# Optimization experiments

Hardware: AMD Instinct MI355X
Metric: run time of the kernel (lower is better)

The kernel has to match this reference:

```python
import jax, jax.numpy as jnp
import numpy as np

HEAD_SIZE = 64

def setup_inputs() -> dict:
    key = jax.random.key(0)
    k1, k2, k3, k4 = jax.random.split(key, 4)
    B, T, D = 4, 4096, 768
    x = jax.random.normal(k1, (B, T, D), dtype=jnp.float32)
    Wq = jax.random.normal(k2, (D, HEAD_SIZE), dtype=jnp.float32) * (1.0 / np.sqrt(D))
    Wk = jax.random.normal(k3, (D, HEAD_SIZE), dtype=jnp.float32) * (1.0 / np.sqrt(D))
    Wv = jax.random.normal(k4, (D, HEAD_SIZE), dtype=jnp.float32) * (1.0 / np.sqrt(D))
    return {"x": x, "Wq": Wq, "Wk": Wk, "Wv": Wv}

def reference(x, Wq, Wk, Wv):
    # q,k,v: [B, T, H]
    q = jnp.einsum('btd,dh->bth', x, Wq)
    k = jnp.einsum('btd,dh->bth', x, Wk)
    v = jnp.einsum('btd,dh->bth', x, Wv)
    # scores: [B, T, T]; causal mask via lower-triangular band, -inf elsewhere
    scores = jnp.einsum('bqh,bkh->bqk', q, k)
    T = x.shape[1]
    causal = jnp.tril(jnp.ones((T, T), dtype=bool))  # band_part(ones, -1, 0)
    scores = jnp.where(causal[None, :, :], scores, -jnp.inf)
    attn = jax.nn.softmax(scores / np.sqrt(HEAD_SIZE), axis=-1)
    # dropout is identity in eval mode
    return jnp.einsum('bqk,bkh->bqh', attn, v)
```

## Files before the change

### kernel.cpp

```cpp
#include <hip/hip_runtime.h>
#include <math.h>

typedef __attribute__((ext_vector_type(8))) short short8;
typedef __attribute__((ext_vector_type(4))) float f32x4;
typedef unsigned short ushort_t;

#define TSEQ   4096
#define NBATCH 4
#define DMODEL 768
#define HS     64

static __device__ __forceinline__ ushort_t f2bf(float f) {
  union { float f; unsigned u; } v; v.f = f;
  unsigned r = v.u + 0x7fffu + ((v.u >> 16) & 1u);
  return (ushort_t)(r >> 16);
}
static __device__ __forceinline__ float bf2f(ushort_t u) {
  union { unsigned u; float f; } v; v.u = ((unsigned)u) << 16; return v.f;
}

#define MFMA16(a,b,c) __builtin_amdgcn_mfma_f32_16x16x32_bf16((a),(b),(c),0,0,0)

__global__ __launch_bounds__(256) void wprep(
    const float* __restrict__ Wq, const float* __restrict__ Wk,
    const float* __restrict__ Wv, ushort_t* __restrict__ Wt)
{
  __shared__ float lds[64 * 65];
  const int m = blockIdx.x / 12, kc = blockIdx.x % 12, k0 = kc * 64;
  const float* W = (m == 0) ? Wq : (m == 1) ? Wk : Wv;
  const int tid = threadIdx.x;
#pragma unroll
  for (int i = 0; i < 16; i++) {
    const int row = i * 4 + (tid >> 6), col = tid & 63;
    lds[row * 65 + col] = W[(size_t)(k0 + row) * HS + col];
  }
  __syncthreads();
#pragma unroll
  for (int i = 0; i < 16; i++) {
    const int n = i * 4 + (tid >> 6), kk = tid & 63;
    Wt[(size_t)(m * 64 + n) * DMODEL + k0 + kk] = f2bf(lds[kk * 65 + n]);
  }
}

__global__ __launch_bounds__(512) void qkv_mfma(
    const float* __restrict__ x, const ushort_t* __restrict__ Wt,
    ushort_t* __restrict__ q, ushort_t* __restrict__ kO, ushort_t* __restrict__ vT)
{
  __shared__ __align__(16) ushort_t Abuf[2][64 * 72];

  const int tid  = threadIdx.x;
  const int w    = tid >> 6, lane = tid & 63;
  const int l16  = lane & 15, quad = lane >> 4;
  const int mh   = w >> 1, ns = w & 1;
  const int M0   = blockIdx.x * 64;
  const float* xg = x + (size_t)M0 * DMODEL;

  const int srow = tid >> 3, scol = (tid & 7) * 8;
  const float* xs = xg + (size_t)srow * DMODEL + scol;
  const ushort_t* wb = Wt + (size_t)(ns * 96 + l16) * DMODEL + quad * 8;

  f32x4 acc[6];
#pragma unroll
  for (int nt = 0; nt < 6; nt++) acc[nt] = (f32x4){0.f, 0.f, 0.f, 0.f};

  float4 pr0 = *(const float4*)(xs);
  float4 pr1 = *(const float4*)(xs + 4);
  short8 bpre[12];
#pragma unroll
  for (int nt = 0; nt < 6; nt++)
#pragma unroll
    for (int kc = 0; kc < 2; kc++)
      bpre[nt * 2 + kc] = *(const short8*)(wb + (size_t)nt * 16 * DMODEL + kc * 32);

  for (int ks = 0; ks < DMODEL / 64; ks++) {
    ushort_t* Ab = &Abuf[ks & 1][0];
    {
      short8 p;
      p[0]=f2bf(pr0.x); p[1]=f2bf(pr0.y); p[2]=f2bf(pr0.z); p[3]=f2bf(pr0.w);
      p[4]=f2bf(pr1.x); p[5]=f2bf(pr1.y); p[6]=f2bf(pr1.z); p[7]=f2bf(pr1.w);
      *(short8*)(Ab + srow * 72 + scol) = p;
    }
    if (ks < DMODEL / 64 - 1) {
      const float* xn = xs + (ks + 1) * 64;
      pr0 = *(const float4*)(xn);
      pr1 = *(const float4*)(xn + 4);
    }
    __syncthreads();
    short8 bcur[12];
#pragma unroll
    for (int t = 0; t < 12; t++) bcur[t] = bpre[t];
    if (ks < DMODEL / 64 - 1) {
#pragma unroll
      for (int nt = 0; nt < 6; nt++)
#pragma unroll
        for (int kc = 0; kc < 2; kc++)
          bpre[nt * 2 + kc] =
              *(const short8*)(wb + (size_t)nt * 16 * DMODEL + (ks + 1) * 64 + kc * 32);
    }
#pragma unroll
    for (int kc = 0; kc < 2; kc++) {
      const short8 af = *(const short8*)(Ab + (mh * 16 + l16) * 72 + kc * 32 + quad * 8);
#pragma unroll
      for (int nt = 0; nt < 6; nt++) acc[nt] = MFMA16(af, bcur[nt * 2 + kc], acc[nt]);
    }
  }

#pragma unroll
  for (int nt = 0; nt < 6; nt++) {
    const int gnt = ns * 6 + nt;
    const int mat = gnt >> 2;
    if (mat <= 1) {
      const int col = (gnt & 3) * 16 + l16;
#pragma unroll
      for (int r = 0; r < 4; r++) {
        const float val = acc[nt][r];
        const int trow = M0 + mh * 16 + quad * 4 + r;
        if (mat == 0) q [(size_t)trow * HS + col] = f2bf(val * 0.125f);
        else          kO[(size_t)trow * HS + col] = f2bf(val);
      }
    }
  }
  __syncthreads();
  float* vls = (float*)&Abuf[0][0];
  if (ns == 1) {
#pragma unroll
    for (int nt = 2; nt < 6; nt++) {
      const int vcol = ((ns * 6 + nt) & 3) * 16 + l16;
#pragma unroll
      for (int r = 0; r < 4; r++)
        vls[(mh * 16 + quad * 4 + r) * 65 + vcol] = acc[nt][r];
    }
  }
  __syncthreads();
  const int d = tid >> 3, seg = tid & 7;
  short8 pk;
#pragma unroll
  for (int i = 0; i < 8; i++) pk[i] = (short)f2bf(vls[(seg * 8 + i) * 65 + d]);
  *(short8*)(vT + ((size_t)(M0 >> 12) * HS + d) * TSEQ + (M0 & (TSEQ - 1)) + seg * 8) = pk;
}

#define KP 72
__global__ __launch_bounds__(128) void attn_part(
    const ushort_t* __restrict__ q, const ushort_t* __restrict__ k,
    const ushort_t* __restrict__ vT, float* __restrict__ ML, ushort_t* __restrict__ OP)
{
  __shared__ __align__(16) ushort_t sK[64 * KP];
  __shared__ __align__(16) ushort_t sV[64 * KP];
  __shared__ __align__(16) ushort_t sP[2][16 * KP];

  const int idx  = blockIdx.x;
  const int s    = idx & 1;
  const int b    = (idx >> 1) & 3;
  const int jt   = 127 - (idx >> 3);
  const int tid  = threadIdx.x;
  const int w    = tid >> 6;
  const int lane = tid & 63;
  const int l16  = lane & 15, quad = lane >> 4;
  const int R0   = jt * 32 + w * 16;

  const ushort_t* qg = q  + (size_t)b * TSEQ * HS;
  const ushort_t* kg = k  + (size_t)b * TSEQ * HS;
  const ushort_t* vg = vT + (size_t)b * HS * TSEQ;

  const short8 qf0 = *(const short8*)(qg + (R0 + l16) * HS +      quad * 8);
  const short8 qf1 = *(const short8*)(qg + (R0 + l16) * HS + 32 + quad * 8);

  f32x4 o[4];
#pragma unroll
  for (int dt = 0; dt < 4; dt++) o[dt] = (f32x4){0.f, 0.f, 0.f, 0.f};
  float mrow = -INFINITY, lrow = 0.f;

  const int nkt = jt / 2 + 1;
  short8 kpre[4], vpre[4];
  int kt = s;
  if (kt < nkt) {
    const int k0 = kt * 64;
#pragma unroll
    for (int i = 0; i < 4; i++) {
      const int c = i * 128 + tid, key = c >> 3, ch = c & 7;
      kpre[i] = *(const short8*)(kg + (size_t)(k0 + key) * HS + ch * 8);
      vpre[i] = *(const short8*)(vg + (size_t)key * TSEQ + k0 + ch * 8);
    }
  }
  for (; kt < nkt; kt += 2) {
    const int k0 = kt * 64;
    __syncthreads();
#pragma unroll
    for (int i = 0; i < 4; i++) {
      const int c = i * 128 + tid, key = c >> 3, ch = c & 7;
      *(short8*)(sK + key * KP + ch * 8) = kpre[i];
      *(short8*)(sV + key * KP + ch * 8) = vpre[i];
    }
    if (kt + 2 < nkt) {
      const int kn = (kt + 2) * 64;
#pragma unroll
      for (int i = 0; i < 4; i++) {
        const int c = i * 128 + tid, key = c >> 3, ch = c & 7;
        kpre[i] = *(const short8*)(kg + (size_t)(kn + key) * HS + ch * 8);
        vpre[i] = *(const short8*)(vg + (size_t)key * TSEQ + kn + ch * 8);
      }
    }
    __syncthreads();
    f32x4 sT[4];
#pragma unroll
    for (int ct = 0; ct < 4; ct++) {
      sT[ct] = (f32x4){0.f, 0.f, 0.f, 0.f};
      const short8 kfa = *(const short8*)(sK + (ct * 16 + l16) * KP +      quad * 8);
      const short8 kfb = *(const short8*)(sK + (ct * 16 + l16) * KP + 32 + quad * 8);
      sT[ct] = MFMA16(kfa, qf0, sT[ct]);
      sT[ct] = MFMA16(kfb, qf1, sT[ct]);
    }
    if (k0 + 63 > R0) {
      const int qrow = R0 + l16;
#pragma unroll
      for (int ct = 0; ct < 4; ct++)
#pragma unroll
        for (int r = 0; r < 4; r++)
          sT[ct][r] = (k0 + ct * 16 + quad * 4 + r <= qrow) ? sT[ct][r] : -INFINITY;
    }
    float tm = -INFINITY;
#pragma unroll
    for (int ct = 0; ct < 4; ct++)
#pragma unroll
      for (int r = 0; r < 4; r++) tm = fmaxf(tm, sT[ct][r]);
    tm = fmaxf(tm, __shfl_xor(tm, 16));
    tm = fmaxf(tm, __shfl_xor(tm, 32));
    const float mn = fmaxf(mrow, tm);
    const float al = __expf(mrow - mn);
    mrow = mn;
    float ps = 0.f;
#pragma unroll
    for (int ct = 0; ct < 4; ct++)
#pragma unroll
      for (int r = 0; r < 4; r++) { sT[ct][r] = __expf(sT[ct][r] - mn); ps += sT[ct][r]; }
    ps += __shfl_xor(ps, 16);
    ps += __shfl_xor(ps, 32);
    lrow = lrow * al + ps;
    ushort_t* Pw = &sP[w][0];
#pragma unroll
    for (int ct = 0; ct < 4; ct++) {
      ushort4 pk;
      pk.x = f2bf(sT[ct][0]); pk.y = f2bf(sT[ct][1]);
      pk.z = f2bf(sT[ct][2]); pk.w = f2bf(sT[ct][3]);
      *(ushort4*)(Pw + l16 * KP + ct * 16 + quad * 4) = pk;
    }
    float alo[4];
#pragma unroll
    for (int r = 0; r < 4; r++) alo[r] = __shfl(al, quad * 4 + r);
#pragma unroll
    for (int dt = 0; dt < 4; dt++)
#pragma unroll
      for (int r = 0; r < 4; r++) o[dt][r] *= alo[r];
    const short8 pf0 = *(const short8*)(Pw + l16 * KP +      quad * 8);
    const short8 pf1 = *(const short8*)(Pw + l16 * KP + 32 + quad * 8);
#pragma unroll
    for (int dt = 0; dt < 4; dt++) {
      const short8 vfa = *(const short8*)(sV + (dt * 16 + l16) * KP +      quad * 8);
      const short8 vfb = *(const short8*)(sV + (dt * 16 + l16) * KP + 32 + quad * 8);
      o[dt] = MFMA16(pf0, vfa, o[dt]);
      o[dt] = MFMA16(pf1, vfb, o[dt]);
    }
  }

  const size_t base = ((size_t)(b * 2 + s) * TSEQ);
  if (quad == 0) {
    ML[(base + R0 + l16) * 2 + 0] = mrow;
    ML[(base + R0 + l16) * 2 + 1] = lrow;
  }
#pragma unroll
  for (int dt = 0; dt < 4; dt++)
#pragma unroll
    for (int r = 0; r < 4; r++)
      OP[(base + R0 + quad * 4 + r) * HS + dt * 16 + l16] = f2bf(o[dt][r]);
}

__global__ __launch_bounds__(256) void attn_merge(
    const float* __restrict__ ML, const ushort_t* __restrict__ OP,
    float* __restrict__ out)
{
  const int row = blockIdx.x * 16 + (threadIdx.x >> 4);
  const int b   = row >> 12, t = row & (TSEQ - 1);
  const int d0  = (threadIdx.x & 15) * 4;
  const size_t i0 = ((size_t)(b * 2 + 0) * TSEQ + t);
  const size_t i1 = ((size_t)(b * 2 + 1) * TSEQ + t);
  const float m0 = ML[i0 * 2], l0 = ML[i0 * 2 + 1];
  const float m1 = ML[i1 * 2], l1 = ML[i1 * 2 + 1];
  const float M  = fmaxf(m0, m1);
  const float a0 = __expf(m0 - M), a1 = __expf(m1 - M);
  const float inv = 1.f / (l0 * a0 + l1 * a1);
  const ushort4 u0 = *(const ushort4*)(OP + i0 * HS + d0);
  const ushort4 u1 = *(const ushort4*)(OP + i1 * HS + d0);
  float4 res;
  res.x = (a0 * bf2f(u0.x) + a1 * bf2f(u1.x)) * inv;
  res.y = (a0 * bf2f(u0.y) + a1 * bf2f(u1.y)) * inv;
  res.z = (a0 * bf2f(u0.z) + a1 * bf2f(u1.z)) * inv;
  res.w = (a0 * bf2f(u0.w) + a1 * bf2f(u1.w)) * inv;
  *(float4*)(out + (size_t)row * HS + d0) = res;
}

extern "C" void kernel_launch(void* const* d_in, const int* in_sizes, int n_in,
                              void* d_out, int out_size, void* d_ws, size_t ws_size,
                              hipStream_t stream) {
  const float* x  = (const float*)d_in[0];
  const float* Wq = (const float*)d_in[1];
  const float* Wk = (const float*)d_in[2];
  const float* Wv = (const float*)d_in[3];
  float* out = (float*)d_out;

  char* ws = (char*)d_ws;
  ushort_t* Wt = (ushort_t*)ws;
  ushort_t* qb = (ushort_t*)(ws + 294912);
  ushort_t* kb = (ushort_t*)(ws + 294912 + 2097152);
  ushort_t* vb = (ushort_t*)(ws + 294912 + 2 * 2097152);
  float*    ml = (float*)   (ws + 294912 + 3 * 2097152);
  ushort_t* op = (ushort_t*)(ws + 294912 + 3 * 2097152 + 262144);

  wprep<<<36, 256, 0, stream>>>(Wq, Wk, Wv, Wt);
  qkv_mfma<<<(NBATCH * TSEQ) / 64, 512, 0, stream>>>(x, Wt, qb, kb, vb);
  attn_part<<<1024, 128, 0, stream>>>(qb, kb, vb, ml, op);
  attn_merge<<<1024, 256, 0, stream>>>(ml, op, out);
}
```

Before: 158.8 us.

## Increase attention key-split to four and halve QKV projection tile

The attention partial kernel now splits each query tile's key range four ways instead of two, launching twice as many blocks and widening the merge step to combine four partial (m, l, O) results. The QKV projection kernel uses 32-row tiles with 256 threads and a two-blocks-per-CU launch bound, doubling its grid. The aim is more parallelism and less tail imbalance in the causal attention pass. In exchange it writes and reads more partial output and adds merge traffic.

```diff
diff --git a/kernel.cpp b/kernel.cpp
--- a/kernel.cpp
+++ b/kernel.cpp
@@ -9,6 +9,7 @@
 #define NBATCH 4
 #define DMODEL 768
 #define HS     64
+#define KSPLIT 4
 
 static __device__ __forceinline__ ushort_t f2bf(float f) {
   union { float f; unsigned u; } v; v.f = f;
@@ -42,17 +43,17 @@
   }
 }
 
-__global__ __launch_bounds__(512) void qkv_mfma(
+__global__ __launch_bounds__(256, 2) void qkv_mfma(
     const float* __restrict__ x, const ushort_t* __restrict__ Wt,
     ushort_t* __restrict__ q, ushort_t* __restrict__ kO, ushort_t* __restrict__ vT)
 {
-  __shared__ __align__(16) ushort_t Abuf[2][64 * 72];
+  __shared__ __align__(16) ushort_t Abuf[2][32 * 72];
 
   const int tid  = threadIdx.x;
   const int w    = tid >> 6, lane = tid & 63;
   const int l16  = lane & 15, quad = lane >> 4;
   const int mh   = w >> 1, ns = w & 1;
-  const int M0   = blockIdx.x * 64;
+  const int M0   = blockIdx.x * 32;
   const float* xg = x + (size_t)M0 * DMODEL;
 
   const int srow = tid >> 3, scol = (tid & 7) * 8;
@@ -132,7 +133,7 @@
     }
   }
   __syncthreads();
-  const int d = tid >> 3, seg = tid & 7;
+  const int d = tid >> 2, seg = tid & 3;
   short8 pk;
 #pragma unroll
   for (int i = 0; i < 8; i++) pk[i] = (short)f2bf(vls[(seg * 8 + i) * 65 + d]);
@@ -149,9 +150,9 @@
   __shared__ __align__(16) ushort_t sP[2][16 * KP];
 
   const int idx  = blockIdx.x;
-  const int s    = idx & 1;
-  const int b    = (idx >> 1) & 3;
-  const int jt   = 127 - (idx >> 3);
+  const int s    = idx & 3;
+  const int b    = (idx >> 2) & 3;
+  const int jt   = 127 - (idx >> 4);
   const int tid  = threadIdx.x;
   const int w    = tid >> 6;
   const int lane = tid & 63;
@@ -182,7 +183,7 @@
       vpre[i] = *(const short8*)(vg + (size_t)key * TSEQ + k0 + ch * 8);
     }
   }
-  for (; kt < nkt; kt += 2) {
+  for (; kt < nkt; kt += KSPLIT) {
     const int k0 = kt * 64;
     __syncthreads();
 #pragma unroll
@@ -191,8 +192,8 @@
       *(short8*)(sK + key * KP + ch * 8) = kpre[i];
       *(short8*)(sV + key * KP + ch * 8) = vpre[i];
     }
-    if (kt + 2 < nkt) {
-      const int kn = (kt + 2) * 64;
+    if (kt + KSPLIT < nkt) {
+      const int kn = (kt + KSPLIT) * 64;
 #pragma unroll
       for (int i = 0; i < 4; i++) {
         const int c = i * 128 + tid, key = c >> 3, ch = c & 7;
@@ -262,7 +263,7 @@
     }
   }
 
-  const size_t base = ((size_t)(b * 2 + s) * TSEQ);
+  const size_t base = ((size_t)(b * KSPLIT + s) * TSEQ);
   if (quad == 0) {
     ML[(base + R0 + l16) * 2 + 0] = mrow;
     ML[(base + R0 + l16) * 2 + 1] = lrow;
@@ -281,21 +282,28 @@
   const int row = blockIdx.x * 16 + (threadIdx.x >> 4);
   const int b   = row >> 12, t = row & (TSEQ - 1);
   const int d0  = (threadIdx.x & 15) * 4;
-  const size_t i0 = ((size_t)(b * 2 + 0) * TSEQ + t);
-  const size_t i1 = ((size_t)(b * 2 + 1) * TSEQ + t);
-  const float m0 = ML[i0 * 2], l0 = ML[i0 * 2 + 1];
-  const float m1 = ML[i1 * 2], l1 = ML[i1 * 2 + 1];
-  const float M  = fmaxf(m0, m1);
-  const float a0 = __expf(m0 - M), a1 = __expf(m1 - M);
-  const float inv = 1.f / (l0 * a0 + l1 * a1);
-  const ushort4 u0 = *(const ushort4*)(OP + i0 * HS + d0);
-  const ushort4 u1 = *(const ushort4*)(OP + i1 * HS + d0);
-  float4 res;
-  res.x = (a0 * bf2f(u0.x) + a1 * bf2f(u1.x)) * inv;
-  res.y = (a0 * bf2f(u0.y) + a1 * bf2f(u1.y)) * inv;
-  res.z = (a0 * bf2f(u0.z) + a1 * bf2f(u1.z)) * inv;
-  res.w = (a0 * bf2f(u0.w) + a1 * bf2f(u1.w)) * inv;
-  *(float4*)(out + (size_t)row * HS + d0) = res;
+  float m[KSPLIT], l[KSPLIT];
+  float M = -INFINITY;
+#pragma unroll
+  for (int ss = 0; ss < KSPLIT; ss++) {
+    const size_t i = ((size_t)(b * KSPLIT + ss) * TSEQ + t);
+    m[ss] = ML[i * 2]; l[ss] = ML[i * 2 + 1];
+    M = fmaxf(M, m[ss]);
+  }
+  float den = 0.f;
+  float4 num = make_float4(0.f, 0.f, 0.f, 0.f);
+#pragma unroll
+  for (int ss = 0; ss < KSPLIT; ss++) {
+    const float a = __expf(m[ss] - M);
+    den += l[ss] * a;
+    const size_t i = ((size_t)(b * KSPLIT + ss) * TSEQ + t);
+    const ushort4 u = *(const ushort4*)(OP + i * HS + d0);
+    num.x += a * bf2f(u.x); num.y += a * bf2f(u.y);
+    num.z += a * bf2f(u.z); num.w += a * bf2f(u.w);
+  }
+  const float inv = 1.f / den;
+  *(float4*)(out + (size_t)row * HS + d0) =
+      make_float4(num.x * inv, num.y * inv, num.z * inv, num.w * inv);
 }
 
 extern "C" void kernel_launch(void* const* d_in, const int* in_sizes, int n_in,
@@ -313,10 +321,10 @@
   ushort_t* kb = (ushort_t*)(ws + 294912 + 2097152);
   ushort_t* vb = (ushort_t*)(ws + 294912 + 2 * 2097152);
   float*    ml = (float*)   (ws + 294912 + 3 * 2097152);
-  ushort_t* op = (ushort_t*)(ws + 294912 + 3 * 2097152 + 262144);
+  ushort_t* op = (ushort_t*)(ws + 294912 + 3 * 2097152 + 524288);
 
   wprep<<<36, 256, 0, stream>>>(Wq, Wk, Wv, Wt);
-  qkv_mfma<<<(NBATCH * TSEQ) / 64, 512, 0, stream>>>(x, Wt, qb, kb, vb);
-  attn_part<<<1024, 128, 0, stream>>>(qb, kb, vb, ml, op);
+  qkv_mfma<<<(NBATCH * TSEQ) / 32, 256, 0, stream>>>(x, Wt, qb, kb, vb);
+  attn_part<<<128 * NBATCH * KSPLIT, 128, 0, stream>>>(qb, kb, vb, ml, op);
   attn_merge<<<1024, 256, 0, stream>>>(ml, op, out);
 }
```

After: 148.7 us. 1.07x faster.
